# Kernel optimization log

Hardware: AMD Instinct MI355X
Metric: run time of the kernel (lower is better)

## Reference

```python
import jax, jax.numpy as jnp
import numpy as np
import math

N_HEAD = 16
D_MODEL = 1024
D_HEAD = 64
GRID = 28


def _alibi_slopes(heads):
    def pow2(n):
        start = 2 ** (-(2 ** (-(math.log2(n) - 3))))
        return [start * (start ** i) for i in range(n)]
    if math.log2(heads).is_integer():
        return pow2(heads)
    c = 2 ** math.floor(math.log2(heads))
    return pow2(c) + pow2(2 * c)[0::2][: heads - c]


def _teeth_bias(heads):
    # bias[i,j] = |i%14 - j%14| + |i//14 - j//14| (loop in get_bias overwrites the -|j-i| init)
    idx = np.arange(GRID)
    row, col = idx // 14, idx % 14
    b = np.abs(col[:, None] - col[None, :]) + np.abs(row[:, None] - row[None, :])  # [28,28]
    slopes = np.asarray(_alibi_slopes(heads), dtype=np.float32)  # [h]
    return jnp.asarray(slopes[:, None, None] * b[None].astype(np.float32))  # [h,28,28]


def _layer_norm(x, gamma, beta, eps=1e-5):
    mu = jnp.mean(x, axis=-1, keepdims=True)
    var = jnp.var(x, axis=-1, keepdims=True)
    return (x - mu) * jax.lax.rsqrt(var + eps) * gamma + beta


def setup_inputs() -> dict:
    key = jax.random.key(0)
    ks = jax.random.split(key, 6)
    s = 0.02
    return {
        "hidden": jax.random.normal(ks[0], (2048, GRID, D_MODEL), dtype=jnp.float32),
        "wq": jax.random.normal(ks[1], (D_MODEL, N_HEAD * D_HEAD), dtype=jnp.float32) * s,
        "wk": jax.random.normal(ks[2], (D_MODEL, N_HEAD * D_HEAD), dtype=jnp.float32) * s,
        "wv": jax.random.normal(ks[3], (D_MODEL, N_HEAD * D_HEAD), dtype=jnp.float32) * s,
        "wo": jax.random.normal(ks[4], (N_HEAD * D_HEAD, D_MODEL), dtype=jnp.float32) * s,
        "gamma": jnp.ones((D_MODEL,), dtype=jnp.float32),
        "beta": jnp.zeros((D_MODEL,), dtype=jnp.float32),
    }


def reference(hidden, wq, wk, wv, wo, gamma, beta):
    b, s, _ = hidden.shape
    # pre_lnorm: hidden is reassigned to LN(hidden); combined == hidden (memory=None)
    h = _layer_norm(hidden, gamma, beta)
    q = (h @ wq).reshape(b, s, N_HEAD, D_HEAD).transpose(0, 2, 1, 3)  # [b,h,s,d]
    k = (h @ wk).reshape(b, s, N_HEAD, D_HEAD).transpose(0, 2, 1, 3)
    v = (h @ wv).reshape(b, s, N_HEAD, D_HEAD).transpose(0, 2, 1, 3)
    # NOTE: original forward never applies atten_scale -> unscaled dots (faithful)
    scores = jnp.einsum("bhid,bhjd->bhij", q, k)
    scores = scores + _teeth_bias(N_HEAD)[None, :, :s, :s]
    attn = jax.nn.softmax(scores, axis=-1)
    ctx = jnp.einsum("bhij,bhjd->bhid", attn, v)
    ctx = ctx.transpose(0, 2, 1, 3).reshape(b, s, N_HEAD * D_HEAD)
    out = ctx @ wo
    return h + out  # pre_lnorm residual uses the normalized hidden
```

## Files before the change

### kernel.cpp

```cpp
#include <hip/hip_runtime.h>
#include <hip/hip_bf16.h>

typedef unsigned short u16;
typedef __attribute__((ext_vector_type(8))) short bf16x8;
typedef __attribute__((ext_vector_type(4))) float f32x4;

#define DEVINL __device__ __forceinline__

DEVINL u16 f2b(float f) {
    __hip_bfloat16 h = __float2bfloat16(f);
    return __builtin_bit_cast(u16, h);
}
DEVINL float b2f(u16 u) {
    unsigned int x = ((unsigned int)u) << 16;
    return __builtin_bit_cast(float, x);
}
DEVINL int iabs(int x) { return x < 0 ? -x : x; }
DEVINL f32x4 MFMA(bf16x8 a, bf16x8 b, f32x4 c) {
    return __builtin_amdgcn_mfma_f32_16x16x32_bf16(a, b, c, 0, 0, 0);
}

#define GL2LDS(g, s)                                                                     \
    __builtin_amdgcn_global_load_lds(                                                    \
        (const __attribute__((address_space(1))) unsigned int*)(g),                      \
        (__attribute__((address_space(3))) unsigned int*)(s), 16, 0, 0)

__global__ __launch_bounds__(256) void wconv_kernel(const float* __restrict__ wq,
                                                    const float* __restrict__ wk,
                                                    const float* __restrict__ wv,
                                                    const float* __restrict__ wo,
                                                    u16* __restrict__ wqkvt,
                                                    u16* __restrict__ wot) {
    __shared__ float tile[32][33];
    int z = blockIdx.z;
    const float* src = (z == 0) ? wq : (z == 1) ? wk : (z == 2) ? wv : wo;
    int n0 = blockIdx.x * 32, k0 = blockIdx.y * 32;
    int r0 = threadIdx.x >> 5, c = threadIdx.x & 31;
#pragma unroll
    for (int i = 0; i < 4; i++) {
        int r = r0 + i * 8;
        tile[r][c] = src[(size_t)(k0 + r) * 1024 + n0 + c];
    }
    __syncthreads();
    u16* dst = (z < 3) ? (wqkvt + (size_t)z * 1024 * 1024) : wot;
#pragma unroll
    for (int i = 0; i < 4; i++) {
        int r = r0 + i * 8;
        dst[(size_t)(n0 + r) * 1024 + k0 + c] = f2b(tile[c][r]);
    }
}

__global__ __launch_bounds__(256) void ln_kernel(const float* __restrict__ x,
                                                 const float* __restrict__ gamma,
                                                 const float* __restrict__ beta,
                                                 u16* __restrict__ h) {
    int w = threadIdx.x >> 6, l = threadIdx.x & 63;
    size_t row = (size_t)blockIdx.x * 4 + w;
    const float4* xr = (const float4*)(x + row * 1024);
    float4 v[4];
    float s = 0.f, sq = 0.f;
#pragma unroll
    for (int i = 0; i < 4; i++) {
        v[i] = xr[l + i * 64];
        s += v[i].x + v[i].y + v[i].z + v[i].w;
        sq += v[i].x * v[i].x + v[i].y * v[i].y + v[i].z * v[i].z + v[i].w * v[i].w;
    }
#pragma unroll
    for (int off = 1; off < 64; off <<= 1) {
        s += __shfl_xor(s, off);
        sq += __shfl_xor(sq, off);
    }
    float mu = s * (1.f / 1024.f);
    float var = sq * (1.f / 1024.f) - mu * mu;
    float rstd = rsqrtf(var + 1e-5f);
    const float4* g4 = (const float4*)gamma;
    const float4* b4 = (const float4*)beta;
#pragma unroll
    for (int i = 0; i < 4; i++) {
        float4 g = g4[l + i * 64], b = b4[l + i * 64];
        float y0 = (v[i].x - mu) * rstd * g.x + b.x;
        float y1 = (v[i].y - mu) * rstd * g.y + b.y;
        float y2 = (v[i].z - mu) * rstd * g.z + b.z;
        float y3 = (v[i].w - mu) * rstd * g.w + b.w;
        unsigned int lo = (unsigned int)f2b(y0) | ((unsigned int)f2b(y1) << 16);
        unsigned int hi = (unsigned int)f2b(y2) | ((unsigned int)f2b(y3) << 16);
        uint2 pk;
        pk.x = lo;
        pk.y = hi;
        *(uint2*)(h + row * 1024 + (size_t)(l + i * 64) * 4) = pk;
    }
}

template <int OUT_BF16, int RESID>
__global__ __launch_bounds__(512, 2) void gemm8(const u16* __restrict__ A,
                                                const u16* __restrict__ Bt,
                                                void* __restrict__ Cv,
                                                const u16* __restrict__ resid,
                                                int lda, int ldc) {
    __shared__ u16 smem[65536];
    int t = threadIdx.x;

    int nwg = gridDim.x;
    int cpx = nwg >> 3;
    int wg = ((int)blockIdx.x & 7) * cpx + ((int)blockIdx.x >> 3);
    int sn = wg / 896;
    int rem = wg - sn * 896;
    int bm = rem >> 2;
    int bn = sn * 4 + (rem & 3);

    int p16 = t * 16;
    int srow = p16 >> 7;
    int scolb = (p16 & 127) ^ ((srow & 7) << 4);
    const char* aP = (const char*)A + (size_t)(bm * 256 + srow) * ((size_t)lda * 2) + scolb;
    const char* bP = (const char*)Bt + (size_t)(bn * 256 + srow) * 2048 + scolb;
    const size_t aStep = (size_t)lda * 2 * 64;
    const size_t bStep = (size_t)2048 * 64;
    char* sbase = (char*)smem;

    int l = t & 63, w = t >> 6;
    int wm = w >> 2, wn = w & 3, g = l >> 4, lr = l & 15;
    int swz = (lr & 7) << 4;
    int ldsoff = lr * 128 + ((g * 16) ^ swz);

    f32x4 acc[8][4];
#pragma unroll
    for (int m = 0; m < 8; m++)
#pragma unroll
        for (int n = 0; n < 4; n++) acc[m][n] = {0.f, 0.f, 0.f, 0.f};

#pragma unroll
    for (int i = 0; i < 4; i++) GL2LDS(aP + i * aStep, sbase + i * 8192 + p16);
#pragma unroll
    for (int i = 0; i < 4; i++) GL2LDS(bP + i * bStep, sbase + 32768 + i * 8192 + p16);
    __syncthreads();

#pragma unroll 1
    for (int tk = 0; tk < 16; ++tk) {
        const char* sA = sbase + (tk & 1) * 65536;
        const char* sAw = sA + wm * 16384;
        const char* sBw = sA + 32768 + wn * 8192;
        char* sd = sbase + ((tk & 1) ^ 1) * 65536;
        size_t kb = (size_t)(tk + 1) * 128;
        bool st = tk < 15;

        bf16x8 af[4][2], b0[2][2], b1[2][2];

#pragma unroll
        for (int m = 0; m < 4; m++)
#pragma unroll
            for (int ks = 0; ks < 2; ks++)
                af[m][ks] = *(const bf16x8*)(sAw + m * 2048 + (ldsoff ^ (ks << 6)));
#pragma unroll
        for (int n = 0; n < 2; n++)
#pragma unroll
            for (int ks = 0; ks < 2; ks++)
                b0[n][ks] = *(const bf16x8*)(sBw + n * 2048 + (ldsoff ^ (ks << 6)));
        if (st) {
            GL2LDS(aP + kb, sd + p16);
            GL2LDS(aP + aStep + kb, sd + 8192 + p16);
        }
        __builtin_amdgcn_s_setprio(1);
#pragma unroll
        for (int m = 0; m < 4; m++)
#pragma unroll
            for (int n = 0; n < 2; n++)
#pragma unroll
                for (int ks = 0; ks < 2; ks++)
                    acc[m][n] = MFMA(af[m][ks], b0[n][ks], acc[m][n]);
        __builtin_amdgcn_s_setprio(0);

#pragma unroll
        for (int n = 0; n < 2; n++)
#pragma unroll
            for (int ks = 0; ks < 2; ks++)
                b1[n][ks] = *(const bf16x8*)(sBw + 4096 + n * 2048 + (ldsoff ^ (ks << 6)));
        if (st) {
            GL2LDS(aP + 2 * aStep + kb, sd + 16384 + p16);
            GL2LDS(aP + 3 * aStep + kb, sd + 24576 + p16);
        }
        __builtin_amdgcn_s_setprio(1);
#pragma unroll
        for (int m = 0; m < 4; m++)
#pragma unroll
            for (int n = 0; n < 2; n++)
#pragma unroll
                for (int ks = 0; ks < 2; ks++)
                    acc[m][2 + n] = MFMA(af[m][ks], b1[n][ks], acc[m][2 + n]);
        __builtin_amdgcn_s_setprio(0);

#pragma unroll
        for (int m = 0; m < 4; m++)
#pragma unroll
            for (int ks = 0; ks < 2; ks++)
                af[m][ks] = *(const bf16x8*)(sAw + 8192 + m * 2048 + (ldsoff ^ (ks << 6)));
        if (st) {
            GL2LDS(bP + kb, sd + 32768 + p16);
            GL2LDS(bP + bStep + kb, sd + 40960 + p16);
        }
        __builtin_amdgcn_s_setprio(1);
#pragma unroll
        for (int m = 0; m < 4; m++)
#pragma unroll
            for (int n = 0; n < 2; n++)
#pragma unroll
                for (int ks = 0; ks < 2; ks++)
                    acc[4 + m][2 + n] = MFMA(af[m][ks], b1[n][ks], acc[4 + m][2 + n]);
        __builtin_amdgcn_s_setprio(0);

        if (st) {
            GL2LDS(bP + 2 * bStep + kb, sd + 49152 + p16);
            GL2LDS(bP + 3 * bStep + kb, sd + 57344 + p16);
        }
        __builtin_amdgcn_s_setprio(1);
#pragma unroll
        for (int m = 0; m < 4; m++)
#pragma unroll
            for (int n = 0; n < 2; n++)
#pragma unroll
                for (int ks = 0; ks < 2; ks++)
                    acc[4 + m][n] = MFMA(af[m][ks], b0[n][ks], acc[4 + m][n]);
        __builtin_amdgcn_s_setprio(0);

        __syncthreads();
    }

    int row0 = bm * 256 + wm * 128;
    int col0 = bn * 256 + wn * 64;
    if (OUT_BF16) {
        u16* C = (u16*)Cv;
#pragma unroll
        for (int qm = 0; qm < 2; qm++)
#pragma unroll
            for (int m = 0; m < 4; m++)
#pragma unroll
                for (int qn = 0; qn < 2; qn++)
#pragma unroll
                    for (int n = 0; n < 2; n++)
#pragma unroll
                        for (int r = 0; r < 4; r++) {
                            size_t rr = (size_t)(row0 + qm * 64 + m * 16 + g * 4 + r);
                            int cc = col0 + qn * 32 + n * 16 + lr;
                            C[rr * (size_t)ldc + cc] = f2b(acc[qm * 4 + m][qn * 2 + n][r]);
                        }
    } else {
        float* C = (float*)Cv;
#pragma unroll
        for (int qm = 0; qm < 2; qm++)
#pragma unroll
            for (int m = 0; m < 4; m++)
#pragma unroll
                for (int qn = 0; qn < 2; qn++)
#pragma unroll
                    for (int n = 0; n < 2; n++)
#pragma unroll
                        for (int r = 0; r < 4; r++) {
                            size_t rr = (size_t)(row0 + qm * 64 + m * 16 + g * 4 + r);
                            int cc = col0 + qn * 32 + n * 16 + lr;
                            float o = acc[qm * 4 + m][qn * 2 + n][r];
                            if (RESID) o += b2f(resid[rr * 1024 + cc]);
                            C[rr * (size_t)ldc + cc] = o;
                        }
    }
}

__global__ __launch_bounds__(256) void attn_kernel(u16* __restrict__ qkv) {
    __shared__ u16 sq[32][264];
    __shared__ u16 sk[32][264];
    __shared__ u16 svt[256][40];
    __shared__ u16 sp[4][32][40];

    int t = threadIdx.x;
    int b = blockIdx.x >> 2, hg = blockIdx.x & 3;
    u16* base = qkv + (size_t)b * 28 * 3072 + hg * 256;

    {
        int rhalf = t >> 7;
        int c2 = (t & 127) * 2;
        for (int it = 0; it < 14; ++it) {
            int row = it * 2 + rhalf;
            const u16* src = base + (size_t)row * 3072;
            unsigned int qv = *(const unsigned int*)(src + c2);
            *(unsigned int*)&sq[row][c2] = qv;
            unsigned int kv = *(const unsigned int*)(src + 1024 + c2);
            *(unsigned int*)&sk[row][c2] = kv;
            unsigned int vv = *(const unsigned int*)(src + 2048 + c2);
            svt[c2][row] = (u16)(vv & 0xffffu);
            svt[c2 + 1][row] = (u16)(vv >> 16);
        }
#pragma unroll
        for (int r = 28; r < 32; ++r) {
            sq[r][t] = 0;
            sk[r][t] = 0;
        }
#pragma unroll
        for (int j = 28; j < 32; ++j) svt[t][j] = 0;
    }
    __syncthreads();

    int w = t >> 6, l = t & 63, g = l >> 4, lr = l & 15;
    int head = hg * 4 + w;

    f32x4 acc[2][2];
#pragma unroll
    for (int a = 0; a < 2; a++)
#pragma unroll
        for (int c = 0; c < 2; c++) acc[a][c] = {0.f, 0.f, 0.f, 0.f};
#pragma unroll
    for (int c = 0; c < 2; c++) {
        int d0 = w * 64 + c * 32 + g * 8;
        bf16x8 a0 = *(const bf16x8*)&sq[lr][d0];
        bf16x8 a1 = *(const bf16x8*)&sq[16 + lr][d0];
        bf16x8 b0 = *(const bf16x8*)&sk[lr][d0];
        bf16x8 b1 = *(const bf16x8*)&sk[16 + lr][d0];
        acc[0][0] = MFMA(a0, b0, acc[0][0]);
        acc[0][1] = MFMA(a0, b1, acc[0][1]);
        acc[1][0] = MFMA(a1, b0, acc[1][0]);
        acc[1][1] = MFMA(a1, b1, acc[1][1]);
    }

    float slope = exp2f(-0.5f * (float)(head + 1));
    int j0 = lr, j1 = 16 + lr;
    int j0m = j0 % 14, j0d = j0 / 14;
    int j1m = j1 % 14, j1d = j1 / 14;
#pragma unroll
    for (int it = 0; it < 2; ++it) {
#pragma unroll
        for (int r = 0; r < 4; ++r) {
            int i = it * 16 + g * 4 + r;
            int im = i % 14, id = i / 14;
            float s0 = acc[it][0][r] + slope * (float)(iabs(im - j0m) + iabs(id - j0d));
            float s1 = (j1 < 28)
                           ? acc[it][1][r] + slope * (float)(iabs(im - j1m) + iabs(id - j1d))
                           : -1e30f;
            float mx = fmaxf(s0, s1);
#pragma unroll
            for (int off = 1; off < 16; off <<= 1) mx = fmaxf(mx, __shfl_xor(mx, off));
            float e0 = __expf(s0 - mx), e1 = __expf(s1 - mx);
            float sm = e0 + e1;
#pragma unroll
            for (int off = 1; off < 16; off <<= 1) sm += __shfl_xor(sm, off);
            float inv = 1.f / sm;
            sp[w][i][lr] = f2b(e0 * inv);
            sp[w][i][16 + lr] = f2b(e1 * inv);
        }
    }
    __syncthreads();

    bf16x8 pa0 = *(const bf16x8*)&sp[w][lr][g * 8];
    bf16x8 pa1 = *(const bf16x8*)&sp[w][16 + lr][g * 8];
    f32x4 o[2][4];
#pragma unroll
    for (int a = 0; a < 2; a++)
#pragma unroll
        for (int d = 0; d < 4; d++) o[a][d] = {0.f, 0.f, 0.f, 0.f};
#pragma unroll
    for (int dt = 0; dt < 4; ++dt) {
        bf16x8 bv = *(const bf16x8*)&svt[w * 64 + dt * 16 + lr][g * 8];
        o[0][dt] = MFMA(pa0, bv, o[0][dt]);
        o[1][dt] = MFMA(pa1, bv, o[1][dt]);
    }
#pragma unroll
    for (int it = 0; it < 2; ++it)
#pragma unroll
        for (int dt = 0; dt < 4; ++dt)
#pragma unroll
            for (int r = 0; r < 4; ++r) {
                int i = it * 16 + g * 4 + r;
                if (i < 28) {
                    size_t off = (size_t)(b * 28 + i) * 3072 + hg * 256 + w * 64 + dt * 16 + lr;
                    qkv[off] = f2b(o[it][dt][r]);
                }
            }
}

extern "C" void kernel_launch(void* const* d_in, const int* in_sizes, int n_in,
                              void* d_out, int out_size, void* d_ws, size_t ws_size,
                              hipStream_t stream) {
    (void)in_sizes; (void)n_in; (void)out_size; (void)ws_size;
    const float* hidden = (const float*)d_in[0];
    const float* wq = (const float*)d_in[1];
    const float* wk = (const float*)d_in[2];
    const float* wv = (const float*)d_in[3];
    const float* wo = (const float*)d_in[4];
    const float* gamma = (const float*)d_in[5];
    const float* beta = (const float*)d_in[6];
    float* out = (float*)d_out;

    char* ws = (char*)d_ws;
    u16* h = (u16*)ws;
    u16* qkv = (u16*)(ws + 117440512);
    u16* wqkvt = (u16*)(ws + 117440512 + 352321536);
    u16* wot = (u16*)(ws + 117440512 + 352321536 + 6291456);

    wconv_kernel<<<dim3(32, 32, 4), 256, 0, stream>>>(wq, wk, wv, wo, wqkvt, wot);
    ln_kernel<<<14336, 256, 0, stream>>>(hidden, gamma, beta, h);
    gemm8<1, 0><<<224 * 12, 512, 0, stream>>>(h, wqkvt, qkv, nullptr, 1024, 3072);
    attn_kernel<<<8192, 256, 0, stream>>>(qkv);
    gemm8<0, 1><<<224 * 4, 512, 0, stream>>>(qkv, wot, out, h, 3072, 1024);
}
```

Measured before the change: 708.7 us.

## Restructure GEMM main loop into 4-stage half-K LDS ring with explicit waitcnt

The GEMM mainloop moves from a double-buffered 128-wide K tile to a ring of four 64-wide K half-tiles for A and B. Global-to-LDS prefetches are issued further ahead, with explicit vmcnt waits, barriers and lgkmcnt fences between MFMA phases. The LDS swizzle changes to match the 64-wide row layout. The goal is deeper load/compute overlap and less time stalled on full-block syncs. In exchange there are more barriers per iteration and a harder-to-verify ordering of asynchronous loads.

```diff
diff --git a/kernel.cpp b/kernel.cpp
--- a/kernel.cpp
+++ b/kernel.cpp
@@ -24,6 +24,12 @@
     __builtin_amdgcn_global_load_lds(                                                    \
         (const __attribute__((address_space(1))) unsigned int*)(g),                      \
         (__attribute__((address_space(3))) unsigned int*)(s), 16, 0, 0)
+
+#define BAR __builtin_amdgcn_s_barrier()
+#define LGKM0                                                                            \
+    asm volatile("s_waitcnt lgkmcnt(0)" ::: "memory");                                   \
+    __builtin_amdgcn_sched_barrier(0)
+#define VMCNT(n) asm volatile("s_waitcnt vmcnt(" #n ")" ::: "memory")
 
 __global__ __launch_bounds__(256) void wconv_kernel(const float* __restrict__ wq,
                                                     const float* __restrict__ wk,
@@ -98,6 +104,7 @@
                                                 const u16* __restrict__ resid,
                                                 int lda, int ldc) {
     __shared__ u16 smem[65536];
+    char* sbase = (char*)smem;
     int t = threadIdx.x;
 
     int nwg = gridDim.x;
@@ -108,19 +115,18 @@
     int bm = rem >> 2;
     int bn = sn * 4 + (rem & 3);
 
+    size_t ldaB = (size_t)lda * 2;
     int p16 = t * 16;
-    int srow = p16 >> 7;
-    int scolb = (p16 & 127) ^ ((srow & 7) << 4);
-    const char* aP = (const char*)A + (size_t)(bm * 256 + srow) * ((size_t)lda * 2) + scolb;
-    const char* bP = (const char*)Bt + (size_t)(bn * 256 + srow) * 2048 + scolb;
-    const size_t aStep = (size_t)lda * 2 * 64;
-    const size_t bStep = (size_t)2048 * 64;
-    char* sbase = (char*)smem;
+    int sr = p16 >> 6;
+    int scb = (p16 & 63) ^ (((p16 >> 7) & 3) << 4);
+    const char* aB = (const char*)A + ((size_t)(bm * 256) + sr) * ldaB + scb;
+    const char* bB = (const char*)Bt + ((size_t)(bn * 256) + sr) * 2048 + scb;
+    const size_t aC = ldaB * 128;
+    const size_t bC = (size_t)2048 * 128;
 
     int l = t & 63, w = t >> 6;
     int wm = w >> 2, wn = w & 3, g = l >> 4, lr = l & 15;
-    int swz = (lr & 7) << 4;
-    int ldsoff = lr * 128 + ((g * 16) ^ swz);
+    int fo = lr * 64 + ((g * 16) ^ (((lr >> 1) & 3) << 4));
 
     f32x4 acc[8][4];
 #pragma unroll
@@ -128,101 +134,118 @@
 #pragma unroll
         for (int n = 0; n < 4; n++) acc[m][n] = {0.f, 0.f, 0.f, 0.f};
 
-#pragma unroll
-    for (int i = 0; i < 4; i++) GL2LDS(aP + i * aStep, sbase + i * 8192 + p16);
-#pragma unroll
-    for (int i = 0; i < 4; i++) GL2LDS(bP + i * bStep, sbase + 32768 + i * 8192 + p16);
-    __syncthreads();
+#define STA(H)                                                                           \
+    do {                                                                                 \
+        size_t ko = (size_t)(((H) >> 1) * 128 + ((H) & 1) * 64);                         \
+        char* d = sbase + ((H) & 3) * 16384 + p16;                                       \
+        GL2LDS(aB + ko, d);                                                              \
+        GL2LDS(aB + aC + ko, d + 8192);                                                  \
+    } while (0)
+#define STB(H)                                                                           \
+    do {                                                                                 \
+        size_t ko = (size_t)(((H) >> 1) * 128 + ((H) & 1) * 64);                         \
+        char* d = sbase + 65536 + ((H) & 3) * 16384 + p16;                               \
+        GL2LDS(bB + ko, d);                                                              \
+        GL2LDS(bB + bC + ko, d + 8192);                                                  \
+    } while (0)
+
+    STA(0); STB(0); STA(1); STB(1); STA(2); STB(2); STA(3);
+    VMCNT(6);
+    BAR;
 
 #pragma unroll 1
-    for (int tk = 0; tk < 16; ++tk) {
-        const char* sA = sbase + (tk & 1) * 65536;
-        const char* sAw = sA + wm * 16384;
-        const char* sBw = sA + 32768 + wn * 8192;
-        char* sd = sbase + ((tk & 1) ^ 1) * 65536;
-        size_t kb = (size_t)(tk + 1) * 128;
-        bool st = tk < 15;
-
-        bf16x8 af[4][2], b0[2][2], b1[2][2];
-
-#pragma unroll
-        for (int m = 0; m < 4; m++)
-#pragma unroll
-            for (int ks = 0; ks < 2; ks++)
-                af[m][ks] = *(const bf16x8*)(sAw + m * 2048 + (ldsoff ^ (ks << 6)));
+    for (int T = 0; T < 16; ++T) {
+        const char* A0 = sbase + ((2 * T) & 3) * 16384;
+        const char* A1 = sbase + ((2 * T + 1) & 3) * 16384;
+        const char* B0 = sbase + 65536 + ((2 * T) & 3) * 16384;
+        const char* B1 = sbase + 65536 + ((2 * T + 1) & 3) * 16384;
+        bf16x8 af[2][4], b0[2], b1[2];
+
+#pragma unroll
+        for (int qm = 0; qm < 2; qm++)
+#pragma unroll
+            for (int m = 0; m < 4; m++)
+                af[qm][m] = *(const bf16x8*)(A0 + (wm * 128 + qm * 64 + m * 16) * 64 + fo);
 #pragma unroll
         for (int n = 0; n < 2; n++)
-#pragma unroll
-            for (int ks = 0; ks < 2; ks++)
-                b0[n][ks] = *(const bf16x8*)(sBw + n * 2048 + (ldsoff ^ (ks << 6)));
-        if (st) {
-            GL2LDS(aP + kb, sd + p16);
-            GL2LDS(aP + aStep + kb, sd + 8192 + p16);
+            b0[n] = *(const bf16x8*)(B0 + (wn * 64 + n * 16) * 64 + fo);
+        if (T < 15) STB(2 * (T + 1) + 1);
+        BAR;
+        LGKM0;
+        __builtin_amdgcn_s_setprio(1);
+#pragma unroll
+        for (int qm = 0; qm < 2; qm++)
+#pragma unroll
+            for (int m = 0; m < 4; m++)
+#pragma unroll
+                for (int n = 0; n < 2; n++)
+                    acc[qm * 4 + m][n] = MFMA(af[qm][m], b0[n], acc[qm * 4 + m][n]);
+        __builtin_amdgcn_s_setprio(0);
+        BAR;
+
+#pragma unroll
+        for (int n = 0; n < 2; n++)
+            b1[n] = *(const bf16x8*)(B0 + (wn * 64 + 32 + n * 16) * 64 + fo);
+        if (T < 14) STA(2 * (T + 2));
+        BAR;
+        LGKM0;
+        __builtin_amdgcn_s_setprio(1);
+#pragma unroll
+        for (int qm = 0; qm < 2; qm++)
+#pragma unroll
+            for (int m = 0; m < 4; m++)
+#pragma unroll
+                for (int n = 0; n < 2; n++)
+                    acc[qm * 4 + m][2 + n] = MFMA(af[qm][m], b1[n], acc[qm * 4 + m][2 + n]);
+        __builtin_amdgcn_s_setprio(0);
+        BAR;
+
+#pragma unroll
+        for (int qm = 0; qm < 2; qm++)
+#pragma unroll
+            for (int m = 0; m < 4; m++)
+                af[qm][m] = *(const bf16x8*)(A1 + (wm * 128 + qm * 64 + m * 16) * 64 + fo);
+#pragma unroll
+        for (int n = 0; n < 2; n++)
+            b0[n] = *(const bf16x8*)(B1 + (wn * 64 + n * 16) * 64 + fo);
+        if (T < 14) STB(2 * (T + 2));
+        BAR;
+        LGKM0;
+        __builtin_amdgcn_s_setprio(1);
+#pragma unroll
+        for (int qm = 0; qm < 2; qm++)
+#pragma unroll
+            for (int m = 0; m < 4; m++)
+#pragma unroll
+                for (int n = 0; n < 2; n++)
+                    acc[qm * 4 + m][n] = MFMA(af[qm][m], b0[n], acc[qm * 4 + m][n]);
+        __builtin_amdgcn_s_setprio(0);
+        BAR;
+
+#pragma unroll
+        for (int n = 0; n < 2; n++)
+            b1[n] = *(const bf16x8*)(B1 + (wn * 64 + 32 + n * 16) * 64 + fo);
+        if (T < 14) STA(2 * (T + 2) + 1);
+        BAR;
+        LGKM0;
+        __builtin_amdgcn_s_setprio(1);
+#pragma unroll
+        for (int qm = 0; qm < 2; qm++)
+#pragma unroll
+            for (int m = 0; m < 4; m++)
+#pragma unroll
+                for (int n = 0; n < 2; n++)
+                    acc[qm * 4 + m][2 + n] = MFMA(af[qm][m], b1[n], acc[qm * 4 + m][2 + n]);
+        __builtin_amdgcn_s_setprio(0);
+        if (T < 14) {
+            VMCNT(6);
+        } else if (T == 14) {
+            VMCNT(0);
         }
-        __builtin_amdgcn_s_setprio(1);
-#pragma unroll
-        for (int m = 0; m < 4; m++)
-#pragma unroll
-            for (int n = 0; n < 2; n++)
-#pragma unroll
-                for (int ks = 0; ks < 2; ks++)
-                    acc[m][n] = MFMA(af[m][ks], b0[n][ks], acc[m][n]);
-        __builtin_amdgcn_s_setprio(0);
-
-#pragma unroll
-        for (int n = 0; n < 2; n++)
-#pragma unroll
-            for (int ks = 0; ks < 2; ks++)
-                b1[n][ks] = *(const bf16x8*)(sBw + 4096 + n * 2048 + (ldsoff ^ (ks << 6)));
-        if (st) {
-            GL2LDS(aP + 2 * aStep + kb, sd + 16384 + p16);
-            GL2LDS(aP + 3 * aStep + kb, sd + 24576 + p16);
-        }
-        __builtin_amdgcn_s_setprio(1);
-#pragma unroll
-        for (int m = 0; m < 4; m++)
-#pragma unroll
-            for (int n = 0; n < 2; n++)
-#pragma unroll
-                for (int ks = 0; ks < 2; ks++)
-                    acc[m][2 + n] = MFMA(af[m][ks], b1[n][ks], acc[m][2 + n]);
-        __builtin_amdgcn_s_setprio(0);
-
-#pragma unroll
-        for (int m = 0; m < 4; m++)
-#pragma unroll
-            for (int ks = 0; ks < 2; ks++)
-                af[m][ks] = *(const bf16x8*)(sAw + 8192 + m * 2048 + (ldsoff ^ (ks << 6)));
-        if (st) {
-            GL2LDS(bP + kb, sd + 32768 + p16);
-            GL2LDS(bP + bStep + kb, sd + 40960 + p16);
-        }
-        __builtin_amdgcn_s_setprio(1);
-#pragma unroll
-        for (int m = 0; m < 4; m++)
-#pragma unroll
-            for (int n = 0; n < 2; n++)
-#pragma unroll
-                for (int ks = 0; ks < 2; ks++)
-                    acc[4 + m][2 + n] = MFMA(af[m][ks], b1[n][ks], acc[4 + m][2 + n]);
-        __builtin_amdgcn_s_setprio(0);
-
-        if (st) {
-            GL2LDS(bP + 2 * bStep + kb, sd + 49152 + p16);
-            GL2LDS(bP + 3 * bStep + kb, sd + 57344 + p16);
-        }
-        __builtin_amdgcn_s_setprio(1);
-#pragma unroll
-        for (int m = 0; m < 4; m++)
-#pragma unroll
-            for (int n = 0; n < 2; n++)
-#pragma unroll
-                for (int ks = 0; ks < 2; ks++)
-                    acc[4 + m][n] = MFMA(af[m][ks], b0[n][ks], acc[4 + m][n]);
-        __builtin_amdgcn_s_setprio(0);
-
-        __syncthreads();
-    }
+        BAR;
+    }
+#undef STA
+#undef STB
 
     int row0 = bm * 256 + wm * 128;
     int col0 = bn * 256 + wn * 64;
```

Result: slower. 753.7 us (+6.3%).
